# Kernel optimization log

Measured on AMD Instinct MI355X. Metric: run time of the kernel, lower is better.

## Reference

```python
import jax, jax.numpy as jnp
import numpy as np

INPUT_DIM = 1024
HEAD_DIM = 64
BATCH = 4
SEQ = 2048


def setup_inputs() -> dict:
    key = jax.random.key(0)
    ks = jax.random.split(key, 7)
    scale = 1.0 / np.sqrt(INPUT_DIM)
    x = jax.random.normal(ks[0], (BATCH, SEQ, INPUT_DIM), dtype=jnp.float32)
    Wq = jax.random.uniform(ks[1], (INPUT_DIM, HEAD_DIM), jnp.float32, -scale, scale)
    bq = jax.random.uniform(ks[2], (HEAD_DIM,), jnp.float32, -scale, scale)
    Wk = jax.random.uniform(ks[3], (INPUT_DIM, HEAD_DIM), jnp.float32, -scale, scale)
    bk = jax.random.uniform(ks[4], (HEAD_DIM,), jnp.float32, -scale, scale)
    Wv = jax.random.uniform(ks[5], (INPUT_DIM, HEAD_DIM), jnp.float32, -scale, scale)
    bv = jax.random.uniform(ks[6], (HEAD_DIM,), jnp.float32, -scale, scale)
    return {"x": x, "Wq": Wq, "bq": bq, "Wk": Wk, "bk": bk, "Wv": Wv, "bv": bv}


def reference(x, Wq, bq, Wk, bk, Wv, bv):
    # q,k,v: [B, S, Hd]
    q = jnp.einsum('bsd,dh->bsh', x, Wq) + bq
    k = jnp.einsum('bsd,dh->bsh', x, Wk) + bk
    v = jnp.einsum('bsd,dh->bsh', x, Wv) + bv
    scores = jnp.einsum('bqh,bkh->bqk', q, k)  # [B, S, S]
    S = scores.shape[-1]
    # causal mask: 0 on/below diagonal, -inf above (matches torch triu().T trick)
    causal = jnp.tril(jnp.ones((S, S), dtype=bool))
    scores = jnp.where(causal, scores, -jnp.inf)
    # original divides by sqrt(head_dim) AFTER adding mask (-inf stays -inf)
    scores = scores / jnp.sqrt(jnp.asarray(q.shape[-1], scores.dtype))
    attn = jax.nn.softmax(scores, axis=-1)
    return jnp.einsum('bqk,bkh->bqh', attn, v)
```

## Files before the change

kernel.cpp:

```cpp
#include <hip/hip_runtime.h>

#define SEQ  2048
#define DIM  1024
#define HD   64

typedef float f32x4  __attribute__((ext_vector_type(4)));
typedef short bf16x8 __attribute__((ext_vector_type(8)));

__device__ __forceinline__ short f2bf(float x) {
    union { float f; unsigned u; } v; v.f = x;
    unsigned r = v.u + 0x7FFFu + ((v.u >> 16) & 1u);
    return (short)(r >> 16);
}
__device__ __forceinline__ short f2bf_fast(float x) {
    union { float f; unsigned u; } v; v.f = x;
    return (short)((v.u + 0x8000u) >> 16);
}

#define MFMA16(a, b, c) __builtin_amdgcn_mfma_f32_16x16x32_bf16((a), (b), (c), 0, 0, 0)

__global__ __launch_bounds__(256) void wprep_kernel(
    const float* __restrict__ Wq, const float* __restrict__ Wk,
    const float* __restrict__ Wv, short* __restrict__ wfrag)
{
    const int idx = blockIdx.x * 256 + threadIdx.x;
    const int l  = idx & 63;
    const int n  = (idx >> 6) & 3;
    const int ks = (idx >> 8) & 31;
    const int w  = idx >> 13;
    const float* __restrict__ W = (w == 0) ? Wq : (w == 1) ? Wk : Wv;
    bf16x8 v;
#pragma unroll
    for (int j = 0; j < 8; ++j)
        v[j] = f2bf(W[(size_t)(ks * 32 + (l >> 4) * 8 + j) * HD + n * 16 + (l & 15)]);
    *reinterpret_cast<bf16x8*>(wfrag + (size_t)idx * 8) = v;
}

__global__ __launch_bounds__(256) void proj_kernel(
    const float* __restrict__ x, const short* __restrict__ wfrag,
    const float* __restrict__ bq, const float* __restrict__ bk,
    const float* __restrict__ bv,
    short* __restrict__ Qs, short* __restrict__ Kb, short* __restrict__ Vt)
{
    __shared__ __align__(16) char smem[49152 + 2304];

    const int tid  = threadIdx.x;
    const int lane = tid & 63;
    const int w    = tid >> 6;
    const int c    = lane & 15;
    const int g    = lane >> 4;
    const int r0   = blockIdx.x * 16;

    f32x4 acc[3][4] = {};
    for (int ks = w * 8; ks < w * 8 + 8; ++ks) {
        const float* xp = x + (size_t)(r0 + c) * DIM + ks * 32 + g * 8;
        float4 a0 = *reinterpret_cast<const float4*>(xp);
        float4 a1 = *reinterpret_cast<const float4*>(xp + 4);
        float av[8] = {a0.x, a0.y, a0.z, a0.w, a1.x, a1.y, a1.z, a1.w};
        bf16x8 af;
#pragma unroll
        for (int j = 0; j < 8; ++j) af[j] = f2bf_fast(av[j]);
#pragma unroll
        for (int which = 0; which < 3; ++which)
#pragma unroll
            for (int n = 0; n < 4; ++n) {
                bf16x8 bfr = *reinterpret_cast<const bf16x8*>(
                    wfrag + ((size_t)((which * 32 + ks) * 4 + n) * 64 + lane) * 8);
                acc[which][n] = MFMA16(af, bfr, acc[which][n]);
            }
    }

    f32x4* red = (f32x4*)smem;
#pragma unroll
    for (int which = 0; which < 3; ++which)
#pragma unroll
        for (int n = 0; n < 4; ++n)
            red[((which * 4 + n) * 4 + w) * 64 + lane] = acc[which][n];
    __syncthreads();

    if (w < 3) {
        const float* __restrict__ bias = (w == 0) ? bq : (w == 1) ? bk : bv;
        f32x4 sum[4];
#pragma unroll
        for (int n = 0; n < 4; ++n) {
            sum[n] = red[((w * 4 + n) * 4 + 0) * 64 + lane];
#pragma unroll
            for (int s = 1; s < 4; ++s)
                sum[n] += red[((w * 4 + n) * 4 + s) * 64 + lane];
        }
        if (w < 2) {
            short* __restrict__ o = (w == 0) ? Qs : Kb;
            const float sc = (w == 0) ? 0.125f : 1.0f;
#pragma unroll
            for (int n = 0; n < 4; ++n) {
                const float bb = bias[n * 16 + c];
#pragma unroll
                for (int i = 0; i < 4; ++i)
                    o[(size_t)(r0 + g * 4 + i) * HD + n * 16 + c] =
                        f2bf((sum[n][i] + bb) * sc);
            }
        } else {
            short* ts = (short*)(smem + 49152);
#pragma unroll
            for (int n = 0; n < 4; ++n) {
                const float bb = bias[n * 16 + c];
#pragma unroll
                for (int i = 0; i < 4; ++i)
                    ts[(g * 4 + i) * 72 + n * 16 + c] = f2bf(sum[n][i] + bb);
            }
            bf16x8 o0, o1;
#pragma unroll
            for (int e = 0; e < 8; ++e) o0[e] = ts[e * 72 + lane];
#pragma unroll
            for (int e = 0; e < 8; ++e) o1[e] = ts[(8 + e) * 72 + lane];
            const int b  = r0 >> 11;
            const int sb = r0 & (SEQ - 1);
            short* dst = Vt + (((size_t)(b * 64 + lane)) << 11) + sb;
            *reinterpret_cast<bf16x8*>(dst)     = o0;
            *reinterpret_cast<bf16x8*>(dst + 8) = o1;
        }
    }
}

__device__ __forceinline__ void tile_step(
    const short* __restrict__ Kb, const short* __restrict__ Vt,
    size_t krow0, int batch, int t, int tlast, int qbase,
    int c, int g, short* P, bf16x8 qf0, bf16x8 qf1,
    f32x4 (&O)[4], float (&m_i)[4], float (&l_i)[4])
{
    const int key0 = t * 64;
    bf16x8 kf[4][2];
#pragma unroll
    for (int n = 0; n < 4; ++n)
#pragma unroll
        for (int st = 0; st < 2; ++st)
            kf[n][st] = *reinterpret_cast<const bf16x8*>(
                Kb + (krow0 + key0 + n * 16 + c) * HD + st * 32 + g * 8);
    f32x4 S[4] = {};
#pragma unroll
    for (int n = 0; n < 4; ++n) {
        S[n] = MFMA16(qf0, kf[n][0], S[n]);
        S[n] = MFMA16(qf1, kf[n][1], S[n]);
    }
    if (t == tlast) {
#pragma unroll
        for (int n = 0; n < 4; ++n)
#pragma unroll
            for (int i = 0; i < 4; ++i)
                if (key0 + n * 16 + c > qbase + g * 4 + i)
                    S[n][i] = -__builtin_inff();
    }
    float mx[4], corr[4], rs[4];
#pragma unroll
    for (int i = 0; i < 4; ++i)
        mx[i] = fmaxf(fmaxf(S[0][i], S[1][i]), fmaxf(S[2][i], S[3][i]));
#pragma unroll
    for (int off = 1; off <= 8; off <<= 1)
#pragma unroll
        for (int i = 0; i < 4; ++i)
            mx[i] = fmaxf(mx[i], __shfl_xor(mx[i], off, 64));
#pragma unroll
    for (int i = 0; i < 4; ++i) {
        const float mn = fmaxf(m_i[i], mx[i]);
        corr[i] = __expf(m_i[i] - mn);
        m_i[i] = mn;
        rs[i] = 0.f;
    }
#pragma unroll
    for (int n = 0; n < 4; ++n)
#pragma unroll
        for (int i = 0; i < 4; ++i) {
            const float p = __expf(S[n][i] - m_i[i]);
            S[n][i] = p;
            rs[i] += p;
        }
#pragma unroll
    for (int off = 1; off <= 8; off <<= 1)
#pragma unroll
        for (int i = 0; i < 4; ++i)
            rs[i] += __shfl_xor(rs[i], off, 64);
#pragma unroll
    for (int i = 0; i < 4; ++i) l_i[i] = l_i[i] * corr[i] + rs[i];
#pragma unroll
    for (int n = 0; n < 4; ++n)
#pragma unroll
        for (int i = 0; i < 4; ++i) O[n][i] *= corr[i];
#pragma unroll
    for (int n = 0; n < 4; ++n)
#pragma unroll
        for (int i = 0; i < 4; ++i)
            P[(g * 4 + i) * 72 + n * 16 + c] = f2bf_fast(S[n][i]);
#pragma unroll
    for (int st = 0; st < 2; ++st) {
        bf16x8 pf = *reinterpret_cast<const bf16x8*>(&P[c * 72 + st * 32 + g * 8]);
#pragma unroll
        for (int n = 0; n < 4; ++n) {
            bf16x8 vf = *reinterpret_cast<const bf16x8*>(
                Vt + (((size_t)(batch * 64 + n * 16 + c)) << 11) + key0 + st * 32 + g * 8);
            O[n] = MFMA16(pf, vf, O[n]);
        }
    }
}

__global__ __launch_bounds__(256) void attn_fused_kernel(
    const short* __restrict__ Qs, const short* __restrict__ Kb,
    const short* __restrict__ Vt, float* __restrict__ out)
{
    __shared__ float  Ost[4][2][16][68];
    __shared__ float2 mlst[4][2][16];
    __shared__ short  Pw[4][16 * 72];

    const int tid  = threadIdx.x;
    const int lane = tid & 63;
    const int w    = tid >> 6;
    const int c    = lane & 15;
    const int g    = lane >> 4;

    const int batch = blockIdx.x >> 6;
    const int p     = blockIdx.x & 63;
    const int qlocA = p;
    const int qlocB = 127 - p;
    const int ntA   = (qlocA >> 2) + 1;
    const int ntB   = (qlocB >> 2) + 1;
    const int qbA   = batch * 128 + qlocA;
    const int qbB   = batch * 128 + qlocB;

    bf16x8 qfA0 = *reinterpret_cast<const bf16x8*>(Qs + (size_t)(qbA * 16 + c) * HD + g * 8);
    bf16x8 qfA1 = *reinterpret_cast<const bf16x8*>(Qs + (size_t)(qbA * 16 + c) * HD + 32 + g * 8);
    bf16x8 qfB0 = *reinterpret_cast<const bf16x8*>(Qs + (size_t)(qbB * 16 + c) * HD + g * 8);
    bf16x8 qfB1 = *reinterpret_cast<const bf16x8*>(Qs + (size_t)(qbB * 16 + c) * HD + 32 + g * 8);

    f32x4 OA[4] = {}, OB[4] = {};
    float mA[4], lA[4], mB[4], lB[4];
#pragma unroll
    for (int i = 0; i < 4; ++i) {
        mA[i] = -__builtin_inff(); lA[i] = 0.f;
        mB[i] = -__builtin_inff(); lB[i] = 0.f;
    }

    short* P = Pw[w];
    const size_t krow0 = (size_t)batch * SEQ;

    for (int idx = w; idx < 33; idx += 4) {
        if (idx < ntA) {
            tile_step(Kb, Vt, krow0, batch, idx, ntA - 1, qlocA * 16,
                      c, g, P, qfA0, qfA1, OA, mA, lA);
        } else {
            tile_step(Kb, Vt, krow0, batch, idx - ntA, ntB - 1, qlocB * 16,
                      c, g, P, qfB0, qfB1, OB, mB, lB);
        }
    }

#pragma unroll
    for (int n = 0; n < 4; ++n)
#pragma unroll
        for (int i = 0; i < 4; ++i) {
            Ost[w][0][g * 4 + i][n * 16 + c] = OA[n][i];
            Ost[w][1][g * 4 + i][n * 16 + c] = OB[n][i];
        }
    if (c == 0) {
#pragma unroll
        for (int i = 0; i < 4; ++i) {
            mlst[w][0][g * 4 + i] = make_float2(mA[i], lA[i]);
            mlst[w][1][g * 4 + i] = make_float2(mB[i], lB[i]);
        }
    }
    __syncthreads();

    {
        const int s  = w >> 1;
        const int qb = (w >> 1) ? qbB : qbA;
#pragma unroll
        for (int ri = 0; ri < 8; ++ri) {
            const int row = (w & 1) * 8 + ri;
            float M = -__builtin_inff();
#pragma unroll
            for (int wv = 0; wv < 4; ++wv)
                M = fmaxf(M, mlst[wv][s][row].x);
            float l = 0.f, o = 0.f;
#pragma unroll
            for (int wv = 0; wv < 4; ++wv) {
                const float2 ml = mlst[wv][s][row];
                const float wgt = __expf(ml.x - M);
                l += wgt * ml.y;
                o += wgt * Ost[wv][s][row][lane];
            }
            out[(size_t)(qb * 16 + row) * HD + lane] = o / l;
        }
    }
}

extern "C" void kernel_launch(void* const* d_in, const int* in_sizes, int n_in,
                              void* d_out, int out_size, void* d_ws, size_t ws_size,
                              hipStream_t stream)
{
    (void)in_sizes; (void)n_in; (void)out_size; (void)ws_size;
    const float* x  = (const float*)d_in[0];
    const float* Wq = (const float*)d_in[1];
    const float* bq = (const float*)d_in[2];
    const float* Wk = (const float*)d_in[3];
    const float* bk = (const float*)d_in[4];
    const float* Wv = (const float*)d_in[5];
    const float* bv = (const float*)d_in[6];
    float* out = (float*)d_out;

    char* ws = (char*)d_ws;
    short* Qs    = (short*)(ws);
    short* Kb    = (short*)(ws + (1u << 20));
    short* Vt    = (short*)(ws + (2u << 20));
    short* wfrag = (short*)(ws + (3u << 20));

    wprep_kernel<<<96, 256, 0, stream>>>(Wq, Wk, Wv, wfrag);
    proj_kernel<<<512, 256, 0, stream>>>(x, wfrag, bq, bk, bv, Qs, Kb, Vt);
    attn_fused_kernel<<<256, 256, 0, stream>>>(Qs, Kb, Vt, out);
}
```

Baseline: 47.47 us.

## Split attention key tiles across eight waves per block instead of four

Doubles the attention block to 512 threads so eight waves share the 33 key tiles of each paired query block, halving the serial tile loop per wave. The cross-wave softmax merge runs twice, once for the A query block and once for the B block, to fit the shared-memory staging into a single-block layout. This adds extra barriers and a longer reduction over eight partial results. It also uses more threads per block with the same 256-block grid.

```diff
diff --git a/kernel.cpp b/kernel.cpp
--- a/kernel.cpp
+++ b/kernel.cpp
@@ -3,6 +3,7 @@
 #define SEQ  2048
 #define DIM  1024
 #define HD   64
+#define AW   8
 
 typedef float f32x4  __attribute__((ext_vector_type(4)));
 typedef short bf16x8 __attribute__((ext_vector_type(8)));
@@ -202,13 +203,13 @@
     }
 }
 
-__global__ __launch_bounds__(256) void attn_fused_kernel(
+__global__ __launch_bounds__(512) void attn_fused_kernel(
     const short* __restrict__ Qs, const short* __restrict__ Kb,
     const short* __restrict__ Vt, float* __restrict__ out)
 {
-    __shared__ float  Ost[4][2][16][68];
-    __shared__ float2 mlst[4][2][16];
-    __shared__ short  Pw[4][16 * 72];
+    __shared__ float  Ost[AW][16][68];
+    __shared__ float2 mlst[AW][16];
+    __shared__ short  Pw[AW][16 * 72];
 
     const int tid  = threadIdx.x;
     const int lane = tid & 63;
@@ -241,7 +242,7 @@
     short* P = Pw[w];
     const size_t krow0 = (size_t)batch * SEQ;
 
-    for (int idx = w; idx < 33; idx += 4) {
+    for (int idx = w; idx < 33; idx += AW) {
         if (idx < ntA) {
             tile_step(Kb, Vt, krow0, batch, idx, ntA - 1, qlocA * 16,
                       c, g, P, qfA0, qfA1, OA, mA, lA);
@@ -254,38 +255,63 @@
 #pragma unroll
     for (int n = 0; n < 4; ++n)
 #pragma unroll
-        for (int i = 0; i < 4; ++i) {
-            Ost[w][0][g * 4 + i][n * 16 + c] = OA[n][i];
-            Ost[w][1][g * 4 + i][n * 16 + c] = OB[n][i];
-        }
+        for (int i = 0; i < 4; ++i)
+            Ost[w][g * 4 + i][n * 16 + c] = OA[n][i];
     if (c == 0) {
 #pragma unroll
-        for (int i = 0; i < 4; ++i) {
-            mlst[w][0][g * 4 + i] = make_float2(mA[i], lA[i]);
-            mlst[w][1][g * 4 + i] = make_float2(mB[i], lB[i]);
-        }
+        for (int i = 0; i < 4; ++i)
+            mlst[w][g * 4 + i] = make_float2(mA[i], lA[i]);
     }
     __syncthreads();
-
     {
-        const int s  = w >> 1;
-        const int qb = (w >> 1) ? qbB : qbA;
-#pragma unroll
-        for (int ri = 0; ri < 8; ++ri) {
-            const int row = (w & 1) * 8 + ri;
+#pragma unroll
+        for (int ri = 0; ri < 2; ++ri) {
+            const int row = w * 2 + ri;
             float M = -__builtin_inff();
 #pragma unroll
-            for (int wv = 0; wv < 4; ++wv)
-                M = fmaxf(M, mlst[wv][s][row].x);
+            for (int wv = 0; wv < AW; ++wv)
+                M = fmaxf(M, mlst[wv][row].x);
             float l = 0.f, o = 0.f;
 #pragma unroll
-            for (int wv = 0; wv < 4; ++wv) {
-                const float2 ml = mlst[wv][s][row];
+            for (int wv = 0; wv < AW; ++wv) {
+                const float2 ml = mlst[wv][row];
                 const float wgt = __expf(ml.x - M);
                 l += wgt * ml.y;
-                o += wgt * Ost[wv][s][row][lane];
-            }
-            out[(size_t)(qb * 16 + row) * HD + lane] = o / l;
+                o += wgt * Ost[wv][row][lane];
+            }
+            out[(size_t)(qbA * 16 + row) * HD + lane] = o / l;
+        }
+    }
+    __syncthreads();
+
+#pragma unroll
+    for (int n = 0; n < 4; ++n)
+#pragma unroll
+        for (int i = 0; i < 4; ++i)
+            Ost[w][g * 4 + i][n * 16 + c] = OB[n][i];
+    if (c == 0) {
+#pragma unroll
+        for (int i = 0; i < 4; ++i)
+            mlst[w][g * 4 + i] = make_float2(mB[i], lB[i]);
+    }
+    __syncthreads();
+    {
+#pragma unroll
+        for (int ri = 0; ri < 2; ++ri) {
+            const int row = w * 2 + ri;
+            float M = -__builtin_inff();
+#pragma unroll
+            for (int wv = 0; wv < AW; ++wv)
+                M = fmaxf(M, mlst[wv][row].x);
+            float l = 0.f, o = 0.f;
+#pragma unroll
+            for (int wv = 0; wv < AW; ++wv) {
+                const float2 ml = mlst[wv][row];
+                const float wgt = __expf(ml.x - M);
+                l += wgt * ml.y;
+                o += wgt * Ost[wv][row][lane];
+            }
+            out[(size_t)(qbB * 16 + row) * HD + lane] = o / l;
         }
     }
 }
@@ -312,5 +338,5 @@
 
     wprep_kernel<<<96, 256, 0, stream>>>(Wq, Wk, Wv, wfrag);
     proj_kernel<<<512, 256, 0, stream>>>(x, wfrag, bq, bk, bv, Qs, Kb, Vt);
-    attn_fused_kernel<<<256, 256, 0, stream>>>(Qs, Kb, Vt, out);
-}
+    attn_fused_kernel<<<256, 512, 0, stream>>>(Qs, Kb, Vt, out);
+}
```

After: 50.06 us. 1.05x slower.

## Process two key tiles per online-softmax step and switch to base-2 exponent

Applied to the files above, without the earlier changes.

Each wave now handles jobs of two 64-key tiles. Both QK^T tiles and all V fragments are loaded up front, and one max/sum reduction and rescale covers 128 keys. This halves the shuffle reductions and correction work per key and exposes more memory-level parallelism. The 1/sqrt(d)*log2(e) factor is folded into Q so exp2f replaces __expf. The cost is higher register use from holding V fragments and S for two tiles, which may reduce occupancy, and the P scratch buffer is widened.

```diff
diff --git a/kernel.cpp b/kernel.cpp
--- a/kernel.cpp
+++ b/kernel.cpp
@@ -3,6 +3,7 @@
 #define SEQ  2048
 #define DIM  1024
 #define HD   64
+#define AW   4
 
 typedef float f32x4  __attribute__((ext_vector_type(4)));
 typedef short bf16x8 __attribute__((ext_vector_type(8)));
@@ -18,6 +19,9 @@
 }
 
 #define MFMA16(a, b, c) __builtin_amdgcn_mfma_f32_16x16x32_bf16((a), (b), (c), 0, 0, 0)
+
+#define QSCALE 0.18033688011f
+#define PSTR   136
 
 __global__ __launch_bounds__(256) void wprep_kernel(
     const float* __restrict__ Wq, const float* __restrict__ Wk,
@@ -90,7 +94,7 @@
         }
         if (w < 2) {
             short* __restrict__ o = (w == 0) ? Qs : Kb;
-            const float sc = (w == 0) ? 0.125f : 1.0f;
+            const float sc = (w == 0) ? QSCALE : 1.0f;
 #pragma unroll
             for (int n = 0; n < 4; ++n) {
                 const float bb = bias[n * 16 + c];
@@ -122,38 +126,65 @@
     }
 }
 
-__device__ __forceinline__ void tile_step(
+template <int WID>
+__device__ __forceinline__ void job_step(
     const short* __restrict__ Kb, const short* __restrict__ Vt,
-    size_t krow0, int batch, int t, int tlast, int qbase,
-    int c, int g, short* P, bf16x8 qf0, bf16x8 qf1,
+    size_t krow0, int batch, int t0, int tlast, int qbase,
+    int c, int g, short* P, bf16x8 q0, bf16x8 q1,
     f32x4 (&O)[4], float (&m_i)[4], float (&l_i)[4])
 {
-    const int key0 = t * 64;
-    bf16x8 kf[4][2];
-#pragma unroll
-    for (int n = 0; n < 4; ++n)
+    f32x4 S[WID][4] = {};
+#pragma unroll
+    for (int tt = 0; tt < WID; ++tt) {
+        const int key0 = (t0 + tt) * 64;
+        bf16x8 kf[4][2];
+#pragma unroll
+        for (int n = 0; n < 4; ++n)
+#pragma unroll
+            for (int st = 0; st < 2; ++st)
+                kf[n][st] = *reinterpret_cast<const bf16x8*>(
+                    Kb + (krow0 + key0 + n * 16 + c) * HD + st * 32 + g * 8);
+#pragma unroll
+        for (int n = 0; n < 4; ++n) {
+            S[tt][n] = MFMA16(q0, kf[n][0], S[tt][n]);
+            S[tt][n] = MFMA16(q1, kf[n][1], S[tt][n]);
+        }
+    }
+
+    bf16x8 vf[WID][2][4];
+#pragma unroll
+    for (int tt = 0; tt < WID; ++tt)
 #pragma unroll
         for (int st = 0; st < 2; ++st)
-            kf[n][st] = *reinterpret_cast<const bf16x8*>(
-                Kb + (krow0 + key0 + n * 16 + c) * HD + st * 32 + g * 8);
-    f32x4 S[4] = {};
-#pragma unroll
-    for (int n = 0; n < 4; ++n) {
-        S[n] = MFMA16(qf0, kf[n][0], S[n]);
-        S[n] = MFMA16(qf1, kf[n][1], S[n]);
-    }
-    if (t == tlast) {
+#pragma unroll
+            for (int n = 0; n < 4; ++n)
+                vf[tt][st][n] = *reinterpret_cast<const bf16x8*>(
+                    Vt + (((size_t)(batch * 64 + n * 16 + c)) << 11)
+                       + (t0 + tt) * 64 + st * 32 + g * 8);
+
+#pragma unroll
+    for (int tt = 0; tt < WID; ++tt) {
+        if (t0 + tt == tlast) {
+            const int key0 = (t0 + tt) * 64;
+#pragma unroll
+            for (int n = 0; n < 4; ++n)
+#pragma unroll
+                for (int i = 0; i < 4; ++i)
+                    if (key0 + n * 16 + c > qbase + g * 4 + i)
+                        S[tt][n][i] = -__builtin_inff();
+        }
+    }
+
+    float mx[4], corr[4], rs[4];
+#pragma unroll
+    for (int i = 0; i < 4; ++i) mx[i] = -__builtin_inff();
+#pragma unroll
+    for (int tt = 0; tt < WID; ++tt)
 #pragma unroll
         for (int n = 0; n < 4; ++n)
 #pragma unroll
             for (int i = 0; i < 4; ++i)
-                if (key0 + n * 16 + c > qbase + g * 4 + i)
-                    S[n][i] = -__builtin_inff();
-    }
-    float mx[4], corr[4], rs[4];
-#pragma unroll
-    for (int i = 0; i < 4; ++i)
-        mx[i] = fmaxf(fmaxf(S[0][i], S[1][i]), fmaxf(S[2][i], S[3][i]));
+                mx[i] = fmaxf(mx[i], S[tt][n][i]);
 #pragma unroll
     for (int off = 1; off <= 8; off <<= 1)
 #pragma unroll
@@ -162,18 +193,20 @@
 #pragma unroll
     for (int i = 0; i < 4; ++i) {
         const float mn = fmaxf(m_i[i], mx[i]);
-        corr[i] = __expf(m_i[i] - mn);
+        corr[i] = exp2f(m_i[i] - mn);
         m_i[i] = mn;
         rs[i] = 0.f;
     }
 #pragma unroll
-    for (int n = 0; n < 4; ++n)
-#pragma unroll
-        for (int i = 0; i < 4; ++i) {
-            const float p = __expf(S[n][i] - m_i[i]);
-            S[n][i] = p;
-            rs[i] += p;
-        }
+    for (int tt = 0; tt < WID; ++tt)
+#pragma unroll
+        for (int n = 0; n < 4; ++n)
+#pragma unroll
+            for (int i = 0; i < 4; ++i) {
+                const float p = exp2f(S[tt][n][i] - m_i[i]);
+                S[tt][n][i] = p;
+                rs[i] += p;
+            }
 #pragma unroll
     for (int off = 1; off <= 8; off <<= 1)
 #pragma unroll
@@ -185,30 +218,33 @@
     for (int n = 0; n < 4; ++n)
 #pragma unroll
         for (int i = 0; i < 4; ++i) O[n][i] *= corr[i];
-#pragma unroll
-    for (int n = 0; n < 4; ++n)
-#pragma unroll
-        for (int i = 0; i < 4; ++i)
-            P[(g * 4 + i) * 72 + n * 16 + c] = f2bf_fast(S[n][i]);
-#pragma unroll
-    for (int st = 0; st < 2; ++st) {
-        bf16x8 pf = *reinterpret_cast<const bf16x8*>(&P[c * 72 + st * 32 + g * 8]);
-#pragma unroll
-        for (int n = 0; n < 4; ++n) {
-            bf16x8 vf = *reinterpret_cast<const bf16x8*>(
-                Vt + (((size_t)(batch * 64 + n * 16 + c)) << 11) + key0 + st * 32 + g * 8);
-            O[n] = MFMA16(pf, vf, O[n]);
-        }
-    }
+
+#pragma unroll
+    for (int tt = 0; tt < WID; ++tt)
+#pragma unroll
+        for (int n = 0; n < 4; ++n)
+#pragma unroll
+            for (int i = 0; i < 4; ++i)
+                P[(g * 4 + i) * PSTR + tt * 64 + n * 16 + c] = f2bf_fast(S[tt][n][i]);
+#pragma unroll
+    for (int tt = 0; tt < WID; ++tt)
+#pragma unroll
+        for (int st = 0; st < 2; ++st) {
+            bf16x8 pf = *reinterpret_cast<const bf16x8*>(
+                &P[c * PSTR + tt * 64 + st * 32 + g * 8]);
+#pragma unroll
+            for (int n = 0; n < 4; ++n)
+                O[n] = MFMA16(pf, vf[tt][st][n], O[n]);
+        }
 }
 
 __global__ __launch_bounds__(256) void attn_fused_kernel(
     const short* __restrict__ Qs, const short* __restrict__ Kb,
     const short* __restrict__ Vt, float* __restrict__ out)
 {
-    __shared__ float  Ost[4][2][16][68];
-    __shared__ float2 mlst[4][2][16];
-    __shared__ short  Pw[4][16 * 72];
+    __shared__ float  Ost[AW][2][16][68];
+    __shared__ float2 mlst[AW][2][16];
+    __shared__ short  Pw[AW][16 * PSTR];
 
     const int tid  = threadIdx.x;
     const int lane = tid & 63;
@@ -241,13 +277,27 @@
     short* P = Pw[w];
     const size_t krow0 = (size_t)batch * SEQ;
 
-    for (int idx = w; idx < 33; idx += 4) {
-        if (idx < ntA) {
-            tile_step(Kb, Vt, krow0, batch, idx, ntA - 1, qlocA * 16,
-                      c, g, P, qfA0, qfA1, OA, mA, lA);
+    const int jobsA = (ntA + 1) >> 1;
+    const int jobsB = (ntB + 1) >> 1;
+    const int NJ    = jobsA + jobsB;
+
+    for (int j = w; j < NJ; j += AW) {
+        if (j < jobsA) {
+            const int t0 = 2 * j;
+            if (t0 + 1 < ntA)
+                job_step<2>(Kb, Vt, krow0, batch, t0, ntA - 1, qlocA * 16,
+                            c, g, P, qfA0, qfA1, OA, mA, lA);
+            else
+                job_step<1>(Kb, Vt, krow0, batch, t0, ntA - 1, qlocA * 16,
+                            c, g, P, qfA0, qfA1, OA, mA, lA);
         } else {
-            tile_step(Kb, Vt, krow0, batch, idx - ntA, ntB - 1, qlocB * 16,
-                      c, g, P, qfB0, qfB1, OB, mB, lB);
+            const int t0 = 2 * (j - jobsA);
+            if (t0 + 1 < ntB)
+                job_step<2>(Kb, Vt, krow0, batch, t0, ntB - 1, qlocB * 16,
+                            c, g, P, qfB0, qfB1, OB, mB, lB);
+            else
+                job_step<1>(Kb, Vt, krow0, batch, t0, ntB - 1, qlocB * 16,
+                            c, g, P, qfB0, qfB1, OB, mB, lB);
         }
     }
 
@@ -275,13 +325,13 @@
             const int row = (w & 1) * 8 + ri;
             float M = -__builtin_inff();
 #pragma unroll
-            for (int wv = 0; wv < 4; ++wv)
+            for (int wv = 0; wv < AW; ++wv)
                 M = fmaxf(M, mlst[wv][s][row].x);
             float l = 0.f, o = 0.f;
 #pragma unroll
-            for (int wv = 0; wv < 4; ++wv) {
+            for (int wv = 0; wv < AW; ++wv) {
                 const float2 ml = mlst[wv][s][row];
-                const float wgt = __expf(ml.x - M);
+                const float wgt = exp2f(ml.x - M);
                 l += wgt * ml.y;
                 o += wgt * Ost[wv][s][row][lane];
             }
```

Result: faster. 46.36 us (-2.3%).
